# Optimization experiments

Hardware: AMD Instinct MI355X
Metric: run time of the kernel (lower is better)

Reference implementation:

```python
import jax, jax.numpy as jnp
import numpy as np

WL_IDX = 0          # water_level_index
THRESH = 0.1        # anomaly threshold
B, T, I, H, O = 2048, 2048, 8, 24, 1


def setup_inputs() -> dict:
    key = jax.random.key(0)
    ks = jax.random.split(key, 7)
    s = float(1.0 / np.sqrt(H))  # PyTorch LSTMCell/Linear uniform init bound
    x = jax.random.normal(ks[0], (B, T, I), dtype=jnp.float32)
    W_ih = jax.random.uniform(ks[1], (4 * H, I), minval=-s, maxval=s, dtype=jnp.float32)
    W_hh = jax.random.uniform(ks[2], (4 * H, H), minval=-s, maxval=s, dtype=jnp.float32)
    b_ih = jax.random.uniform(ks[3], (4 * H,), minval=-s, maxval=s, dtype=jnp.float32)
    b_hh = jax.random.uniform(ks[4], (4 * H,), minval=-s, maxval=s, dtype=jnp.float32)
    W_out = jax.random.uniform(ks[5], (O, H), minval=-s, maxval=s, dtype=jnp.float32)
    b_out = jax.random.uniform(ks[6], (O,), minval=-s, maxval=s, dtype=jnp.float32)
    return {"x": x, "W_ih": W_ih, "W_hh": W_hh, "b_ih": b_ih, "b_hh": b_hh,
            "W_out": W_out, "b_out": b_out}


def reference(x, W_ih, W_hh, b_ih, b_hh, W_out, b_out):
    # x: (B, T, I) -> preds: (B, T, O)
    Bs, Ts, Is = x.shape
    Hs = W_hh.shape[1]
    h0 = jnp.zeros((Bs, Hs), x.dtype)
    c0 = jnp.zeros((Bs, Hs), x.dtype)
    # Init pred equal to t=0 water level -> anomaly flag is False at t=0,
    # reproducing the original's ungated first step.
    pred0 = x[:, 0, WL_IDX:WL_IDX + 1]  # (B, 1)
    xs = jnp.swapaxes(x, 0, 1)  # (T, B, I)

    def step(carry, x_t):
        h, c, pred = carry
        actual = x_t[:, WL_IDX:WL_IDX + 1]            # (B, 1)
        anom = jnp.abs(pred - actual) > THRESH         # (B, 1) bool
        wl = jnp.where(anom[:, 0], pred[:, 0], x_t[:, WL_IDX])
        inp = x_t.at[:, WL_IDX].set(wl)                # anomaly-gated input
        # LSTMCell: gates in PyTorch order i, f, g, o
        gates = inp @ W_ih.T + b_ih + h @ W_hh.T + b_hh  # (B, 4H)
        i_g, f_g, g_g, o_g = jnp.split(gates, 4, axis=1)
        c_new = jax.nn.sigmoid(f_g) * c + jax.nn.sigmoid(i_g) * jnp.tanh(g_g)
        h_new = jax.nn.sigmoid(o_g) * jnp.tanh(c_new)
        pred_new = h_new @ W_out.T + b_out             # (B, O)
        return (h_new, c_new, pred_new), pred_new

    _, preds = jax.lax.scan(step, (h0, c0, pred0), xs)  # (T, B, O)
    return jnp.swapaxes(preds, 0, 1)  # (B, T, O)
```

## Files before the change

kernel.cpp:

```cpp
#include <hip/hip_runtime.h>

#define TT 2048
#define II 8
#define HH 24
#define THRESH 0.1f
#define LOG2E 1.4426950408889634f

#define ROR_ADD(a, N)                                                          \
    {                                                                          \
        int t_ = __builtin_amdgcn_update_dpp(0, __float_as_int(a),             \
                                             0x120 + (N), 0xF, 0xF, false);    \
        (a) += __int_as_float(t_);                                             \
    }

__global__ __launch_bounds__(64, 2)
void lstm_anom_kernel(const float* __restrict__ x,
                      const float* __restrict__ W_ih,
                      const float* __restrict__ W_hh,
                      const float* __restrict__ b_ih,
                      const float* __restrict__ b_hh,
                      const float* __restrict__ W_out,
                      const float* __restrict__ b_out,
                      float* __restrict__ out)
{
    __shared__ __align__(16) float vbuf[32];

    const int  lane  = threadIdx.x;
    const int  b     = blockIdx.x;
    const int  l32   = lane & 31;
    const bool hi    = lane >= 32;
    const bool unitL = (l32 < HH);
    const int  jc    = unitL ? l32 : 0;
    const bool xL    = (!hi) && (l32 >= 24);
    const int  xk    = l32 - 24;

    const float* xb = x + (size_t)b * (TT * II);

    const int rowA = (hi ? 2 * HH : 0) + jc;
    const int rowB = rowA + HH;
    float wA[32], wB[32];
    #pragma unroll
    for (int k = 0; k < II; ++k) {
        wA[k] = W_ih[rowA * II + k];
        wB[k] = W_ih[rowB * II + k];
    }
    #pragma unroll
    for (int k = 0; k < HH; ++k) {
        wA[II + k] = W_hh[rowA * HH + k];
        wB[II + k] = W_hh[rowB * HH + k];
    }
    const float biasA = b_ih[rowA] + b_hh[rowA];
    const float biasB = b_ih[rowB] + b_hh[rowB];
    const float kA = hi ? (-2.f * LOG2E) : (-LOG2E);
    const float mA = hi ? 2.f : 1.f;
    const float nA = hi ? -1.f : 0.f;
    const float woutj = unitL ? W_out[jc] : 0.f;
    const float bout  = b_out[0];

    if (lane < 32) vbuf[lane] = (lane < 8) ? xb[lane] : 0.f;
    float xA = 0.f, xB = 0.f;
    if (xL) xA = xb[II + xk];
    __syncthreads();

    float v[32];
    #pragma unroll
    for (int c8 = 0; c8 < 8; ++c8) {
        const float4 q = *(const float4*)&vbuf[c8 * 4];
        v[c8 * 4 + 0] = q.x; v[c8 * 4 + 1] = q.y;
        v[c8 * 4 + 2] = q.z; v[c8 * 4 + 3] = q.w;
    }
    float pred = v[0];
    float cst = 0.f, predsave = 0.f;

    for (int t = 0; t < TT; ++t) {
        v[0] = (fabsf(pred - v[0]) > THRESH) ? pred : v[0];

        float aA = biasA, aB = biasB;
        #pragma unroll
        for (int k = 0; k < 32; ++k) {
            aA = fmaf(wA[k], v[k], aA);
            aB = fmaf(wB[k], v[k], aB);
        }

        const float sA = __builtin_amdgcn_rcpf(1.f + __builtin_amdgcn_exp2f(kA * aA));
        const float tA = fmaf(sA, mA, nA);
        const float sB = __builtin_amdgcn_rcpf(1.f + __builtin_amdgcn_exp2f(-LOG2E * aB));
        auto rA = __builtin_amdgcn_permlane32_swap(__float_as_int(tA), __float_as_int(tA), false, false);
        auto rB = __builtin_amdgcn_permlane32_swap(__float_as_int(sB), __float_as_int(sB), false, false);
        const float ig = __int_as_float(rA[0]);
        const float gg = __int_as_float(rA[1]);
        const float fg = __int_as_float(rB[0]);
        const float og = __int_as_float(rB[1]);

        cst = fmaf(fg, cst, ig * gg);
        const float sc = __builtin_amdgcn_rcpf(1.f + __builtin_amdgcn_exp2f(-2.f * LOG2E * cst));
        const float tc = fmaf(2.f, sc, -1.f);
        const float h  = og * tc;

        if (lane < 32) vbuf[xL ? xk : (8 + l32)] = xL ? xA : h;
        if (xL) {
            int tn = t + 2; if (tn > TT - 1) tn = TT - 1;
            xB = xb[(size_t)tn * II + xk];
        }

        float p = woutj * h;
        {
            auto r = __builtin_amdgcn_permlane16_swap(__float_as_int(p), __float_as_int(p), false, false);
            p = __int_as_float(r[0]) + __int_as_float(r[1]);
        }
        ROR_ADD(p, 8); ROR_ADD(p, 4); ROR_ADD(p, 2); ROR_ADD(p, 1);
        pred = p + bout;

        predsave = ((t & 63) == lane) ? pred : predsave;
        if ((t & 63) == 63) out[(size_t)b * TT + (t - 63) + lane] = predsave;

        __syncthreads();

        #pragma unroll
        for (int c8 = 0; c8 < 8; ++c8) {
            const float4 q = *(const float4*)&vbuf[c8 * 4];
            v[c8 * 4 + 0] = q.x; v[c8 * 4 + 1] = q.y;
            v[c8 * 4 + 2] = q.z; v[c8 * 4 + 3] = q.w;
        }
        if (xL) xA = xB;
    }
}

extern "C" void kernel_launch(void* const* d_in, const int* in_sizes, int n_in,
                              void* d_out, int out_size, void* d_ws, size_t ws_size,
                              hipStream_t stream) {
    const float* x     = (const float*)d_in[0];
    const float* W_ih  = (const float*)d_in[1];
    const float* W_hh  = (const float*)d_in[2];
    const float* b_ih  = (const float*)d_in[3];
    const float* b_hh  = (const float*)d_in[4];
    const float* W_out = (const float*)d_in[5];
    const float* b_out = (const float*)d_in[6];
    float* out = (float*)d_out;

    dim3 grid(2048);
    dim3 block(64);
    lstm_anom_kernel<<<grid, block, 0, stream>>>(x, W_ih, W_hh, b_ih, b_hh,
                                                 W_out, b_out, out);
}
```

Before: 808.1 us.

## Use packed v_pk_fma for gate dot products and per-lane x prefetch

Repacks the per-lane weights and the input vector into float2 pairs so the 32-term gate dot products run as packed FMAs, halving the FMA instruction count on the serial recurrence. Every lane now loads the next x row directly from global memory as float4s instead of staging it through shared memory, so the LDS buffer holds only h. The __syncthreads is removed, which relies on the single 64-lane wave being in lockstep. This adds two global loads per lane per step and a final add to reduce each packed accumulator.

New measurement: 838.2 us. 3.7% more time.

```diff
diff --git a/kernel.cpp b/kernel.cpp
--- a/kernel.cpp
+++ b/kernel.cpp
@@ -5,6 +5,8 @@
 #define HH 24
 #define THRESH 0.1f
 #define LOG2E 1.4426950408889634f
+
+typedef float v2f __attribute__((ext_vector_type(2)));
 
 #define ROR_ADD(a, N)                                                          \
     {                                                                          \
@@ -31,56 +33,70 @@
     const bool hi    = lane >= 32;
     const bool unitL = (l32 < HH);
     const int  jc    = unitL ? l32 : 0;
-    const bool xL    = (!hi) && (l32 >= 24);
-    const int  xk    = l32 - 24;
 
     const float* xb = x + (size_t)b * (TT * II);
 
     const int rowA = (hi ? 2 * HH : 0) + jc;
     const int rowB = rowA + HH;
-    float wA[32], wB[32];
+    float wAf[32], wBf[32];
     #pragma unroll
     for (int k = 0; k < II; ++k) {
-        wA[k] = W_ih[rowA * II + k];
-        wB[k] = W_ih[rowB * II + k];
+        wAf[k] = W_ih[rowA * II + k];
+        wBf[k] = W_ih[rowB * II + k];
     }
     #pragma unroll
     for (int k = 0; k < HH; ++k) {
-        wA[II + k] = W_hh[rowA * HH + k];
-        wB[II + k] = W_hh[rowB * HH + k];
+        wAf[II + k] = W_hh[rowA * HH + k];
+        wBf[II + k] = W_hh[rowB * HH + k];
     }
-    const float biasA = b_ih[rowA] + b_hh[rowA];
-    const float biasB = b_ih[rowB] + b_hh[rowB];
+    v2f wA2[16], wB2[16];
+    #pragma unroll
+    for (int k = 0; k < 16; ++k) {
+        wA2[k] = (v2f){ wAf[2 * k], wAf[2 * k + 1] };
+        wB2[k] = (v2f){ wBf[2 * k], wBf[2 * k + 1] };
+    }
+    #pragma unroll
+    for (int k = 0; k < 16; ++k) {
+        asm volatile("" : "+v"(wA2[k]));
+        asm volatile("" : "+v"(wB2[k]));
+    }
+    float biasA = b_ih[rowA] + b_hh[rowA];
+    float biasB = b_ih[rowB] + b_hh[rowB];
+    asm volatile("" : "+v"(biasA));
+    asm volatile("" : "+v"(biasB));
     const float kA = hi ? (-2.f * LOG2E) : (-LOG2E);
     const float mA = hi ? 2.f : 1.f;
     const float nA = hi ? -1.f : 0.f;
     const float woutj = unitL ? W_out[jc] : 0.f;
     const float bout  = b_out[0];
 
-    if (lane < 32) vbuf[lane] = (lane < 8) ? xb[lane] : 0.f;
-    float xA = 0.f, xB = 0.f;
-    if (xL) xA = xb[II + xk];
-    __syncthreads();
+    v2f v2r[16];
+    {
+        const float4 q0 = *(const float4*)(xb + 0);
+        const float4 q1 = *(const float4*)(xb + 4);
+        v2r[0] = (v2f){q0.x, q0.y}; v2r[1] = (v2f){q0.z, q0.w};
+        v2r[2] = (v2f){q1.x, q1.y}; v2r[3] = (v2f){q1.z, q1.w};
+    }
+    #pragma unroll
+    for (int k = 4; k < 16; ++k) v2r[k] = (v2f){0.f, 0.f};
+    float4 xn0 = *(const float4*)(xb + II);
+    float4 xn1 = *(const float4*)(xb + II + 4);
 
-    float v[32];
-    #pragma unroll
-    for (int c8 = 0; c8 < 8; ++c8) {
-        const float4 q = *(const float4*)&vbuf[c8 * 4];
-        v[c8 * 4 + 0] = q.x; v[c8 * 4 + 1] = q.y;
-        v[c8 * 4 + 2] = q.z; v[c8 * 4 + 3] = q.w;
-    }
-    float pred = v[0];
+    float pred = v2r[0].x;
     float cst = 0.f, predsave = 0.f;
 
     for (int t = 0; t < TT; ++t) {
-        v[0] = (fabsf(pred - v[0]) > THRESH) ? pred : v[0];
+        v2r[0].x = (fabsf(pred - v2r[0].x) > THRESH) ? pred : v2r[0].x;
 
-        float aA = biasA, aB = biasB;
+        v2f accA = (v2f){biasA, 0.f};
+        v2f accB = (v2f){biasB, 0.f};
         #pragma unroll
-        for (int k = 0; k < 32; ++k) {
-            aA = fmaf(wA[k], v[k], aA);
-            aB = fmaf(wB[k], v[k], aB);
+        for (int k = 0; k < 16; ++k) {
+            accA = __builtin_elementwise_fma(wA2[k], v2r[k], accA);
+            accB = __builtin_elementwise_fma(wB2[k], v2r[k], accB);
         }
+        const float aA = accA.x + accA.y;
+        const float aB = accB.x + accB.y;
 
         const float sA = __builtin_amdgcn_rcpf(1.f + __builtin_amdgcn_exp2f(kA * aA));
         const float tA = fmaf(sA, mA, nA);
@@ -97,11 +113,11 @@
         const float tc = fmaf(2.f, sc, -1.f);
         const float h  = og * tc;
 
-        if (lane < 32) vbuf[xL ? xk : (8 + l32)] = xL ? xA : h;
-        if (xL) {
-            int tn = t + 2; if (tn > TT - 1) tn = TT - 1;
-            xB = xb[(size_t)tn * II + xk];
-        }
+        if (lane < HH) vbuf[lane] = h;
+
+        int tn = t + 2; if (tn > TT - 1) tn = TT - 1;
+        const float4 xp0 = *(const float4*)(xb + (size_t)tn * II);
+        const float4 xp1 = *(const float4*)(xb + (size_t)tn * II + 4);
 
         float p = woutj * h;
         {
@@ -114,15 +130,23 @@
         predsave = ((t & 63) == lane) ? pred : predsave;
         if ((t & 63) == 63) out[(size_t)b * TT + (t - 63) + lane] = predsave;
 
-        __syncthreads();
-
-        #pragma unroll
-        for (int c8 = 0; c8 < 8; ++c8) {
-            const float4 q = *(const float4*)&vbuf[c8 * 4];
-            v[c8 * 4 + 0] = q.x; v[c8 * 4 + 1] = q.y;
-            v[c8 * 4 + 2] = q.z; v[c8 * 4 + 3] = q.w;
+        v2r[0] = (v2f){xn0.x, xn0.y}; v2r[1] = (v2f){xn0.z, xn0.w};
+        v2r[2] = (v2f){xn1.x, xn1.y}; v2r[3] = (v2f){xn1.z, xn1.w};
+        {
+            const float4 h0 = *(const float4*)&vbuf[0];
+            const float4 h1 = *(const float4*)&vbuf[4];
+            const float4 h2 = *(const float4*)&vbuf[8];
+            const float4 h3 = *(const float4*)&vbuf[12];
+            const float4 h4 = *(const float4*)&vbuf[16];
+            const float4 h5 = *(const float4*)&vbuf[20];
+            v2r[4]  = (v2f){h0.x, h0.y}; v2r[5]  = (v2f){h0.z, h0.w};
+            v2r[6]  = (v2f){h1.x, h1.y}; v2r[7]  = (v2f){h1.z, h1.w};
+            v2r[8]  = (v2f){h2.x, h2.y}; v2r[9]  = (v2f){h2.z, h2.w};
+            v2r[10] = (v2f){h3.x, h3.y}; v2r[11] = (v2f){h3.z, h3.w};
+            v2r[12] = (v2f){h4.x, h4.y}; v2r[13] = (v2f){h4.z, h4.w};
+            v2r[14] = (v2f){h5.x, h5.y}; v2r[15] = (v2f){h5.z, h5.w};
         }
-        if (xL) xA = xB;
+        xn0 = xp0; xn1 = xp1;
     }
 }
 
```

## Interleave two batch sequences per wave with split vector accumulators

Applied to the files above, without the earlier changes.

Each 64-lane wave now runs two independent batch recurrences, one per half-wave for the shared-memory state, and interleaves their arithmetic. The grid is halved and one wave per SIMD is forced. The 32-term gate dot product is split into four partial accumulators, which shortens the serial FMA chain, and the per-step __syncthreads is dropped because the block is a single wave. This trades wave-level parallelism for instruction-level parallelism inside one wave. It also changes floating-point summation order slightly.

Result: slower. 913.0 us (+13.0%).

```diff
diff --git a/kernel.cpp b/kernel.cpp
--- a/kernel.cpp
+++ b/kernel.cpp
@@ -6,6 +6,8 @@
 #define THRESH 0.1f
 #define LOG2E 1.4426950408889634f
 
+typedef float v4f __attribute__((ext_vector_type(4)));
+
 #define ROR_ADD(a, N)                                                          \
     {                                                                          \
         int t_ = __builtin_amdgcn_update_dpp(0, __float_as_int(a),             \
@@ -13,7 +15,8 @@
         (a) += __int_as_float(t_);                                             \
     }
 
-__global__ __launch_bounds__(64, 2)
+__global__ __launch_bounds__(64)
+__attribute__((amdgpu_waves_per_eu(1, 1)))
 void lstm_anom_kernel(const float* __restrict__ x,
                       const float* __restrict__ W_ih,
                       const float* __restrict__ W_hh,
@@ -23,31 +26,33 @@
                       const float* __restrict__ b_out,
                       float* __restrict__ out)
 {
-    __shared__ __align__(16) float vbuf[32];
+    __shared__ __align__(16) float vbuf[64];
 
     const int  lane  = threadIdx.x;
-    const int  b     = blockIdx.x;
+    const int  b0    = blockIdx.x * 2;
+    const int  b1    = b0 + 1;
     const int  l32   = lane & 31;
     const bool hi    = lane >= 32;
     const bool unitL = (l32 < HH);
     const int  jc    = unitL ? l32 : 0;
-    const bool xL    = (!hi) && (l32 >= 24);
+    const bool xL    = (l32 >= 24);
     const int  xk    = l32 - 24;
 
-    const float* xb = x + (size_t)b * (TT * II);
+    const float* xb0 = x + (size_t)b0 * (TT * II);
+    const float* xb1 = x + (size_t)b1 * (TT * II);
+    const float* xbs = hi ? xb1 : xb0;
 
     const int rowA = (hi ? 2 * HH : 0) + jc;
     const int rowB = rowA + HH;
-    float wA[32], wB[32];
+    v4f wA4[8], wB4[8];
+    wA4[0] = *(const v4f*)(W_ih + rowA * II);
+    wA4[1] = *(const v4f*)(W_ih + rowA * II + 4);
+    wB4[0] = *(const v4f*)(W_ih + rowB * II);
+    wB4[1] = *(const v4f*)(W_ih + rowB * II + 4);
     #pragma unroll
-    for (int k = 0; k < II; ++k) {
-        wA[k] = W_ih[rowA * II + k];
-        wB[k] = W_ih[rowB * II + k];
-    }
-    #pragma unroll
-    for (int k = 0; k < HH; ++k) {
-        wA[II + k] = W_hh[rowA * HH + k];
-        wB[II + k] = W_hh[rowB * HH + k];
+    for (int q = 0; q < 6; ++q) {
+        wA4[2 + q] = *(const v4f*)(W_hh + rowA * HH + q * 4);
+        wB4[2 + q] = *(const v4f*)(W_hh + rowB * HH + q * 4);
     }
     const float biasA = b_ih[rowA] + b_hh[rowA];
     const float biasB = b_ih[rowB] + b_hh[rowB];
@@ -57,71 +62,90 @@
     const float woutj = unitL ? W_out[jc] : 0.f;
     const float bout  = b_out[0];
 
-    if (lane < 32) vbuf[lane] = (lane < 8) ? xb[lane] : 0.f;
+    vbuf[hi * 32 + l32] = (l32 < 8) ? xbs[l32] : 0.f;
     float xA = 0.f, xB = 0.f;
-    if (xL) xA = xb[II + xk];
-    __syncthreads();
+    if (xL) xA = xbs[II + xk];
 
-    float v[32];
+    const v4f* pv = (const v4f*)vbuf;
+    v4f v0[8], v1[8];
     #pragma unroll
-    for (int c8 = 0; c8 < 8; ++c8) {
-        const float4 q = *(const float4*)&vbuf[c8 * 4];
-        v[c8 * 4 + 0] = q.x; v[c8 * 4 + 1] = q.y;
-        v[c8 * 4 + 2] = q.z; v[c8 * 4 + 3] = q.w;
-    }
-    float pred = v[0];
-    float cst = 0.f, predsave = 0.f;
+    for (int q = 0; q < 8; ++q) { v0[q] = pv[q]; v1[q] = pv[8 + q]; }
+
+    float pred0 = v0[0].x, pred1 = v1[0].x;
+    float cst0 = 0.f, cst1 = 0.f, ps0 = 0.f, ps1 = 0.f;
 
     for (int t = 0; t < TT; ++t) {
-        v[0] = (fabsf(pred - v[0]) > THRESH) ? pred : v[0];
+        v0[0].x = (fabsf(pred0 - v0[0].x) > THRESH) ? pred0 : v0[0].x;
+        v1[0].x = (fabsf(pred1 - v1[0].x) > THRESH) ? pred1 : v1[0].x;
 
-        float aA = biasA, aB = biasB;
+        v4f aA0 = (v4f){biasA, 0.f, 0.f, 0.f};
+        v4f aB0 = (v4f){biasB, 0.f, 0.f, 0.f};
+        v4f aA1 = (v4f){biasA, 0.f, 0.f, 0.f};
+        v4f aB1 = (v4f){biasB, 0.f, 0.f, 0.f};
         #pragma unroll
-        for (int k = 0; k < 32; ++k) {
-            aA = fmaf(wA[k], v[k], aA);
-            aB = fmaf(wB[k], v[k], aB);
+        for (int q = 0; q < 8; ++q) {
+            aA0 = __builtin_elementwise_fma(wA4[q], v0[q], aA0);
+            aB0 = __builtin_elementwise_fma(wB4[q], v0[q], aB0);
+            aA1 = __builtin_elementwise_fma(wA4[q], v1[q], aA1);
+            aB1 = __builtin_elementwise_fma(wB4[q], v1[q], aB1);
+        }
+        const float sA0v = (aA0.x + aA0.y) + (aA0.z + aA0.w);
+        const float sB0v = (aB0.x + aB0.y) + (aB0.z + aB0.w);
+        const float sA1v = (aA1.x + aA1.y) + (aA1.z + aA1.w);
+        const float sB1v = (aB1.x + aB1.y) + (aB1.z + aB1.w);
+
+        const float sA0 = __builtin_amdgcn_rcpf(1.f + __builtin_amdgcn_exp2f(kA * sA0v));
+        const float tA0 = fmaf(sA0, mA, nA);
+        const float sB0 = __builtin_amdgcn_rcpf(1.f + __builtin_amdgcn_exp2f(-LOG2E * sB0v));
+        const float sA1 = __builtin_amdgcn_rcpf(1.f + __builtin_amdgcn_exp2f(kA * sA1v));
+        const float tA1 = fmaf(sA1, mA, nA);
+        const float sB1 = __builtin_amdgcn_rcpf(1.f + __builtin_amdgcn_exp2f(-LOG2E * sB1v));
+
+        auto rA0 = __builtin_amdgcn_permlane32_swap(__float_as_int(tA0), __float_as_int(tA0), false, false);
+        auto rB0 = __builtin_amdgcn_permlane32_swap(__float_as_int(sB0), __float_as_int(sB0), false, false);
+        auto rA1 = __builtin_amdgcn_permlane32_swap(__float_as_int(tA1), __float_as_int(tA1), false, false);
+        auto rB1 = __builtin_amdgcn_permlane32_swap(__float_as_int(sB1), __float_as_int(sB1), false, false);
+        const float ig0 = __int_as_float(rA0[0]), gg0 = __int_as_float(rA0[1]);
+        const float fg0 = __int_as_float(rB0[0]), og0 = __int_as_float(rB0[1]);
+        const float ig1 = __int_as_float(rA1[0]), gg1 = __int_as_float(rA1[1]);
+        const float fg1 = __int_as_float(rB1[0]), og1 = __int_as_float(rB1[1]);
+
+        cst0 = fmaf(fg0, cst0, ig0 * gg0);
+        cst1 = fmaf(fg1, cst1, ig1 * gg1);
+        const float sc0 = __builtin_amdgcn_rcpf(1.f + __builtin_amdgcn_exp2f(-2.f * LOG2E * cst0));
+        const float sc1 = __builtin_amdgcn_rcpf(1.f + __builtin_amdgcn_exp2f(-2.f * LOG2E * cst1));
+        const float h0 = og0 * fmaf(2.f, sc0, -1.f);
+        const float h1 = og1 * fmaf(2.f, sc1, -1.f);
+
+        vbuf[hi * 32 + (xL ? xk : 8 + l32)] = xL ? xA : (hi ? h1 : h0);
+        if (xL) {
+            int tn = t + 2; if (tn > TT - 1) tn = TT - 1;
+            xB = xbs[(size_t)tn * II + xk];
         }
 
-        const float sA = __builtin_amdgcn_rcpf(1.f + __builtin_amdgcn_exp2f(kA * aA));
-        const float tA = fmaf(sA, mA, nA);
-        const float sB = __builtin_amdgcn_rcpf(1.f + __builtin_amdgcn_exp2f(-LOG2E * aB));
-        auto rA = __builtin_amdgcn_permlane32_swap(__float_as_int(tA), __float_as_int(tA), false, false);
-        auto rB = __builtin_amdgcn_permlane32_swap(__float_as_int(sB), __float_as_int(sB), false, false);
-        const float ig = __int_as_float(rA[0]);
-        const float gg = __int_as_float(rA[1]);
-        const float fg = __int_as_float(rB[0]);
-        const float og = __int_as_float(rB[1]);
+        float p0 = woutj * h0, p1 = woutj * h1;
+        {
+            auto r0 = __builtin_amdgcn_permlane16_swap(__float_as_int(p0), __float_as_int(p0), false, false);
+            auto r1 = __builtin_amdgcn_permlane16_swap(__float_as_int(p1), __float_as_int(p1), false, false);
+            p0 = __int_as_float(r0[0]) + __int_as_float(r0[1]);
+            p1 = __int_as_float(r1[0]) + __int_as_float(r1[1]);
+        }
+        ROR_ADD(p0, 8); ROR_ADD(p1, 8);
+        ROR_ADD(p0, 4); ROR_ADD(p1, 4);
+        ROR_ADD(p0, 2); ROR_ADD(p1, 2);
+        ROR_ADD(p0, 1); ROR_ADD(p1, 1);
+        pred0 = p0 + bout;
+        pred1 = p1 + bout;
 
-        cst = fmaf(fg, cst, ig * gg);
-        const float sc = __builtin_amdgcn_rcpf(1.f + __builtin_amdgcn_exp2f(-2.f * LOG2E * cst));
-        const float tc = fmaf(2.f, sc, -1.f);
-        const float h  = og * tc;
-
-        if (lane < 32) vbuf[xL ? xk : (8 + l32)] = xL ? xA : h;
-        if (xL) {
-            int tn = t + 2; if (tn > TT - 1) tn = TT - 1;
-            xB = xb[(size_t)tn * II + xk];
+        ps0 = ((t & 63) == lane) ? pred0 : ps0;
+        ps1 = ((t & 63) == lane) ? pred1 : ps1;
+        if ((t & 63) == 63) {
+            out[(size_t)b0 * TT + (t - 63) + lane] = ps0;
+            out[(size_t)b1 * TT + (t - 63) + lane] = ps1;
         }
 
-        float p = woutj * h;
-        {
-            auto r = __builtin_amdgcn_permlane16_swap(__float_as_int(p), __float_as_int(p), false, false);
-            p = __int_as_float(r[0]) + __int_as_float(r[1]);
-        }
-        ROR_ADD(p, 8); ROR_ADD(p, 4); ROR_ADD(p, 2); ROR_ADD(p, 1);
-        pred = p + bout;
-
-        predsave = ((t & 63) == lane) ? pred : predsave;
-        if ((t & 63) == 63) out[(size_t)b * TT + (t - 63) + lane] = predsave;
-
-        __syncthreads();
-
         #pragma unroll
-        for (int c8 = 0; c8 < 8; ++c8) {
-            const float4 q = *(const float4*)&vbuf[c8 * 4];
-            v[c8 * 4 + 0] = q.x; v[c8 * 4 + 1] = q.y;
-            v[c8 * 4 + 2] = q.z; v[c8 * 4 + 3] = q.w;
-        }
+        for (int q = 0; q < 8; ++q) { v0[q] = pv[q]; v1[q] = pv[8 + q]; }
         if (xL) xA = xB;
     }
 }
@@ -138,7 +162,7 @@
     const float* b_out = (const float*)d_in[6];
     float* out = (float*)d_out;
 
-    dim3 grid(2048);
+    dim3 grid(1024);
     dim3 block(64);
     lstm_anom_kernel<<<grid, block, 0, stream>>>(x, W_ih, W_hh, b_ih, b_hh,
                                                  W_out, b_out, out);
```
